# Performance work log

Hardware: AMD Instinct MI355X
Metric: run time of the kernel (lower is better)

The kernel has to match this reference:

```python
import jax, jax.numpy as jnp
import numpy as np

N = 100000      # nodes
E = 3200000     # edges (avg degree 32)
F_IN = 512      # node features
H = 256         # hidden width (channels[0])
C = 64          # num_classes
K = 10          # APPNP steps
ALPHA = 0.1     # teleport prob


def setup_inputs() -> dict:
    key = jax.random.key(0)
    k1, k2, k3, k4 = jax.random.split(key, 4)
    x = jax.random.normal(k1, (N, F_IN), dtype=jnp.float32)
    edge_index = jax.random.randint(k2, (2, E), 0, N, dtype=jnp.int32)
    W1 = jax.random.normal(k3, (F_IN, H), dtype=jnp.float32) * (1.0 / np.sqrt(F_IN))
    b1 = jnp.zeros((H,), dtype=jnp.float32)
    W2 = jax.random.normal(k4, (H, C), dtype=jnp.float32) * (1.0 / np.sqrt(H))
    b2 = jnp.zeros((C,), dtype=jnp.float32)
    return {"x": x, "edge_index": edge_index, "W1": W1, "b1": b1, "W2": W2, "b2": b2}


def reference(x, edge_index, W1, b1, W2, b2):
    # MLP encoder (dropout is identity at eval time)
    h = jax.nn.relu(x @ W1 + b1) @ W2 + b2  # [N, C]

    # GCN normalization with added self-loops (PyG APPNP default)
    loops = jnp.arange(N, dtype=edge_index.dtype)
    row = jnp.concatenate([edge_index[0], loops])  # source
    col = jnp.concatenate([edge_index[1], loops])  # target
    deg = jax.ops.segment_sum(jnp.ones_like(col, dtype=h.dtype), col, num_segments=N)
    dinv = jnp.where(deg > 0, jax.lax.rsqrt(deg), 0.0)
    norm = (dinv[row] * dinv[col])[:, None]  # [E+N, 1]

    # APPNP: z_{k+1} = (1-alpha) * A_hat z_k + alpha * h
    z = h
    for _ in range(K):
        msg = z[row] * norm                                   # gather + scale
        agg = jax.ops.segment_sum(msg, col, num_segments=N)   # scatter-add
        z = (1.0 - ALPHA) * agg + ALPHA * h

    return jax.nn.log_softmax(z, axis=1)
```

## Files before the change

kernel.cpp:

```cpp
#include <hip/hip_runtime.h>
#include <hip/hip_bf16.h>

#define F_IN 512
#define H_DIM 256
#define C_DIM 64
#define K_STEPS 10
#define ALPHA 0.1f

typedef __attribute__((ext_vector_type(8))) short bf16x8;
typedef __attribute__((ext_vector_type(4))) float f32x4;

static __device__ __forceinline__ ushort f2bf(float f) {
    __hip_bfloat16 b = __float2bfloat16(f);
    return *(ushort*)&b;
}
static __device__ __forceinline__ float bflo(unsigned int w) {
    union { unsigned int i; float f; } v; v.i = w << 16; return v.f;
}
static __device__ __forceinline__ float bfhi(unsigned int w) {
    union { unsigned int i; float f; } v; v.i = w & 0xffff0000u; return v.f;
}

#define ACC8(u) do { \
    acc[0] += bflo(u.x); acc[1] += bfhi(u.x); \
    acc[2] += bflo(u.y); acc[3] += bfhi(u.y); \
    acc[4] += bflo(u.z); acc[5] += bfhi(u.z); \
    acc[6] += bflo(u.w); acc[7] += bfhi(u.w); } while (0)

__global__ void prep_kernel(const float* __restrict__ W1, ushort* __restrict__ W1p,
                            const float* __restrict__ W2, ushort* __restrict__ W2p,
                            int* __restrict__ cnt, int n)
{
    const int o = blockIdx.x * 256 + threadIdx.x;
    {
        const int j = o & 7;
        const int l = (o >> 3) & 63;
        const int b = o >> 9;
        const int f = b & 15, ks = b >> 4;
        const int k = ks * 32 + (l >> 4) * 8 + j;
        const int col = f * 16 + (l & 15);
        W1p[o] = f2bf(W1[k * H_DIM + col]);
    }
    if (o < 16384) {
        const int j = o & 7;
        const int l = (o >> 3) & 63;
        const int b = o >> 9;
        const int f = b & 3, kk = b >> 2;
        const int k = kk * 32 + (l >> 4) * 8 + j;
        const int col = f * 16 + (l & 15);
        W2p[o] = f2bf(W2[k * C_DIM + col]);
    }
    if (o < n) cnt[o] = 0;
}

__global__ void rank_kernel(const int* __restrict__ col, int* __restrict__ cnt,
                            int* __restrict__ rank, int e)
{
    int i = blockIdx.x * 256 + threadIdx.x;
    if (i < e) rank[i] = atomicAdd(&cnt[col[i]], 1);
}

__global__ __launch_bounds__(256) void scan1_kernel(
    const int* __restrict__ cnt, int* __restrict__ rowptr, int* __restrict__ sums,
    float* __restrict__ dinv, int n)
{
    __shared__ int lds[256];
    const int t = threadIdx.x;
    const int base = blockIdx.x * 1024 + t * 4;
    int v[4];
    #pragma unroll
    for (int j = 0; j < 4; ++j) v[j] = (base + j < n) ? cnt[base + j] : 0;
    const int tsum = v[0] + v[1] + v[2] + v[3];
    lds[t] = tsum;
    __syncthreads();
    for (int o = 1; o < 256; o <<= 1) {
        const int add = (t >= o) ? lds[t - o] : 0;
        __syncthreads();
        lds[t] += add;
        __syncthreads();
    }
    int run = lds[t] - tsum;
    #pragma unroll
    for (int j = 0; j < 4; ++j) {
        if (base + j < n) {
            rowptr[base + j] = run;
            dinv[base + j] = rsqrtf((float)v[j] + 1.0f);
        }
        run += v[j];
    }
    if (t == 255) sums[blockIdx.x] = lds[255];
}

__global__ __launch_bounds__(128) void scan2_kernel(int* __restrict__ sums, int nc)
{
    __shared__ int lds[128];
    const int t = threadIdx.x;
    const int v = (t < nc) ? sums[t] : 0;
    lds[t] = v;
    __syncthreads();
    for (int o = 1; o < 128; o <<= 1) {
        const int add = (t >= o) ? lds[t - o] : 0;
        __syncthreads();
        lds[t] += add;
        __syncthreads();
    }
    if (t < nc) sums[t] = lds[t] - v;
}

__global__ void scan3_kernel(int* __restrict__ rowptr, const int* __restrict__ sums, int n, int e)
{
    int i = blockIdx.x * 256 + threadIdx.x;
    if (i < n) rowptr[i] += sums[i >> 10];
    else if (i == n) rowptr[n] = e;
}

__global__ void fill_kernel(const int* __restrict__ row, const int* __restrict__ col,
                            const int* __restrict__ rowptr, const int* __restrict__ rank,
                            int* __restrict__ csr_src, int e)
{
    int i = blockIdx.x * 256 + threadIdx.x;
    if (i < e) csr_src[rowptr[col[i]] + rank[i]] = row[i];
}

__global__ __launch_bounds__(256) void mlp_mfma_kernel(
    const float* __restrict__ x,
    const ushort* __restrict__ W1p, const float* __restrict__ b1,
    const ushort* __restrict__ W2p, const float* __restrict__ b2,
    const float* __restrict__ dinv,
    ushort* __restrict__ ah, ushort* __restrict__ zs, int n)
{
    __shared__ __align__(16) short h1s[4][16 * 264];

    const int t = threadIdx.x;
    const int lane = t & 63;
    const int wv = t >> 6;
    const int ln15 = lane & 15;
    const int hi = lane >> 4;
    const long row0 = (long)blockIdx.x * 64 + wv * 16;

    long arow = row0 + ln15;
    if (arow > (long)n - 1) arow = n - 1;
    const float4* xp = (const float4*)(x + arow * F_IN);

    f32x4 acc[16];
    #pragma unroll
    for (int f = 0; f < 16; ++f) acc[f] = (f32x4){0.f, 0.f, 0.f, 0.f};

    float4 xb[2][2];
    xb[0][0] = xp[hi * 2];     xb[0][1] = xp[hi * 2 + 1];
    xb[1][0] = xp[8 + hi * 2]; xb[1][1] = xp[8 + hi * 2 + 1];

    #pragma unroll
    for (int ks = 0; ks < 16; ++ks) {
        const int sl = ks & 1;
        const float4 a0 = xb[sl][0];
        const float4 a1 = xb[sl][1];
        if (ks + 2 < 16) {
            xb[sl][0] = xp[(ks + 2) * 8 + hi * 2];
            xb[sl][1] = xp[(ks + 2) * 8 + hi * 2 + 1];
        }
        bf16x8 af;
        af[0] = (short)f2bf(a0.x); af[1] = (short)f2bf(a0.y);
        af[2] = (short)f2bf(a0.z); af[3] = (short)f2bf(a0.w);
        af[4] = (short)f2bf(a1.x); af[5] = (short)f2bf(a1.y);
        af[6] = (short)f2bf(a1.z); af[7] = (short)f2bf(a1.w);
        const ushort* wb = W1p + (long)ks * 8192 + lane * 8;
        #pragma unroll
        for (int f = 0; f < 16; ++f) {
            const bf16x8 bfv = *(const bf16x8*)(wb + f * 512);
            acc[f] = __builtin_amdgcn_mfma_f32_16x16x32_bf16(af, bfv, acc[f], 0, 0, 0);
        }
    }

    short* hb = h1s[wv];
    #pragma unroll
    for (int f = 0; f < 16; ++f) {
        const int col = f * 16 + ln15;
        const float bias = b1[col];
        #pragma unroll
        for (int v = 0; v < 4; ++v) {
            float val = acc[f][v] + bias;
            val = val > 0.f ? val : 0.f;
            hb[(hi * 4 + v) * 264 + col] = (short)f2bf(val);
        }
    }

    f32x4 acc2[4];
    #pragma unroll
    for (int f = 0; f < 4; ++f) acc2[f] = (f32x4){0.f, 0.f, 0.f, 0.f};
    #pragma unroll
    for (int kk = 0; kk < 8; ++kk) {
        const bf16x8 a2 = *(const bf16x8*)&hb[ln15 * 264 + kk * 32 + hi * 8];
        #pragma unroll
        for (int f = 0; f < 4; ++f) {
            const bf16x8 b2f = *(const bf16x8*)&W2p[(kk * 4 + f) * 512 + lane * 8];
            acc2[f] = __builtin_amdgcn_mfma_f32_16x16x32_bf16(a2, b2f, acc2[f], 0, 0, 0);
        }
    }

    float di4[4];
    #pragma unroll
    for (int v = 0; v < 4; ++v) {
        const long r = row0 + hi * 4 + v;
        di4[v] = (r < n) ? dinv[r] : 0.f;
    }
    #pragma unroll
    for (int f = 0; f < 4; ++f) {
        const int col = f * 16 + ln15;
        const float bias = b2[col];
        #pragma unroll
        for (int v = 0; v < 4; ++v) {
            const long r = row0 + hi * 4 + v;
            if (r < n) {
                const float val = acc2[f][v] + bias;
                ah[r * C_DIM + col] = f2bf(ALPHA * val);
                zs[r * C_DIM + col] = f2bf(val * di4[v]);
            }
        }
    }
}

__global__ __launch_bounds__(256) void gather8_kernel(
    const int* __restrict__ rowptr, const int* __restrict__ csr_src,
    const float* __restrict__ dinv, const ushort* __restrict__ ah,
    const ushort* __restrict__ zs_in, ushort* __restrict__ zs_out,
    float* __restrict__ out, int n, int final_it)
{
    const int node = (blockIdx.x * 256 + threadIdx.x) >> 6;
    if (node >= n) return;
    const int lane = threadIdx.x & 63;
    const int s = lane >> 3;
    const int cg = lane & 7;

    const int p0 = rowptr[node];
    const int p1 = rowptr[node + 1];

    float acc[8];
    #pragma unroll
    for (int c = 0; c < 8; ++c) acc[c] = 0.f;

    if (s == 0) {
        const uint4 u = *(const uint4*)&zs_in[(long)node * C_DIM + cg * 8];
        ACC8(u);
    }

    if (p0 < p1) {
        int p = p0 + s;
        int c0 = (p     < p1) ? csr_src[p]     : -1;
        int c1 = (p + 8 < p1) ? csr_src[p + 8] : -1;
        while (c0 >= 0) {
            uint4 u0, u1;
            u0 = *(const uint4*)&zs_in[(long)c0 * C_DIM + cg * 8];
            if (c1 >= 0) u1 = *(const uint4*)&zs_in[(long)c1 * C_DIM + cg * 8];
            const int np = p + 16;
            const int n0 = (np     < p1) ? csr_src[np]     : -1;
            const int n1 = (np + 8 < p1) ? csr_src[np + 8] : -1;
            ACC8(u0);
            if (c1 >= 0) ACC8(u1);
            c0 = n0; c1 = n1; p = np;
        }
    }

    #pragma unroll
    for (int c = 0; c < 8; ++c) {
        acc[c] += __shfl_xor(acc[c], 8, 64);
        acc[c] += __shfl_xor(acc[c], 16, 64);
        acc[c] += __shfl_xor(acc[c], 32, 64);
    }

    if (s == 0) {
        const float di = dinv[node];
        const long off = (long)node * C_DIM + cg * 8;
        const uint4 ua = *(const uint4*)&ah[off];
        const float w = (1.0f - ALPHA) * di;
        float z[8];
        z[0] = w * acc[0] + bflo(ua.x);
        z[1] = w * acc[1] + bfhi(ua.x);
        z[2] = w * acc[2] + bflo(ua.y);
        z[3] = w * acc[3] + bfhi(ua.y);
        z[4] = w * acc[4] + bflo(ua.z);
        z[5] = w * acc[5] + bfhi(ua.z);
        z[6] = w * acc[6] + bflo(ua.w);
        z[7] = w * acc[7] + bfhi(ua.w);
        if (!final_it) {
            uint4 o;
            o.x = ((unsigned)f2bf(z[1] * di) << 16) | f2bf(z[0] * di);
            o.y = ((unsigned)f2bf(z[3] * di) << 16) | f2bf(z[2] * di);
            o.z = ((unsigned)f2bf(z[5] * di) << 16) | f2bf(z[4] * di);
            o.w = ((unsigned)f2bf(z[7] * di) << 16) | f2bf(z[6] * di);
            *(uint4*)&zs_out[off] = o;
        } else {
            float m = z[0];
            #pragma unroll
            for (int j = 1; j < 8; ++j) m = fmaxf(m, z[j]);
            m = fmaxf(m, __shfl_xor(m, 1, 64));
            m = fmaxf(m, __shfl_xor(m, 2, 64));
            m = fmaxf(m, __shfl_xor(m, 4, 64));
            float se = 0.f;
            #pragma unroll
            for (int j = 0; j < 8; ++j) se += expf(z[j] - m);
            se += __shfl_xor(se, 1, 64);
            se += __shfl_xor(se, 2, 64);
            se += __shfl_xor(se, 4, 64);
            const float ls = m + logf(se);
            *(float4*)&out[off]     = make_float4(z[0] - ls, z[1] - ls, z[2] - ls, z[3] - ls);
            *(float4*)&out[off + 4] = make_float4(z[4] - ls, z[5] - ls, z[6] - ls, z[7] - ls);
        }
    }
}

extern "C" void kernel_launch(void* const* d_in, const int* in_sizes, int n_in,
                              void* d_out, int out_size, void* d_ws, size_t ws_size,
                              hipStream_t stream)
{
    const float* x  = (const float*)d_in[0];
    const int* ei   = (const int*)d_in[1];
    const float* W1 = (const float*)d_in[2];
    const float* b1 = (const float*)d_in[3];
    const float* W2 = (const float*)d_in[4];
    const float* b2 = (const float*)d_in[5];
    float* out = (float*)d_out;

    const int N = in_sizes[0] / F_IN;
    const int E = in_sizes[1] / 2;
    const int* row = ei;
    const int* col = ei + E;

    ushort* ah     = (ushort*)d_ws;
    ushort* zs_a   = ah + (long)N * C_DIM;
    ushort* zs_b   = zs_a + (long)N * C_DIM;
    float*  dinv   = (float*)(zs_b + (long)N * C_DIM);
    int*    cnt    = (int*)(dinv + N);
    int*    rowptr = cnt + N;
    int*    rank   = rowptr + N + 16;
    int*    csr_src = rank + E;
    int*    sums   = csr_src + E;
    ushort* W1p    = (ushort*)(sums + 128);
    ushort* W2p    = W1p + 131072;

    const int eblk = (E + 255) / 256;
    const int nchunks = (N + 1023) / 1024;

    prep_kernel<<<512, 256, 0, stream>>>(W1, W1p, W2, W2p, cnt, N);

    rank_kernel<<<eblk, 256, 0, stream>>>(col, cnt, rank, E);
    scan1_kernel<<<nchunks, 256, 0, stream>>>(cnt, rowptr, sums, dinv, N);
    scan2_kernel<<<1, 128, 0, stream>>>(sums, nchunks);
    scan3_kernel<<<(N + 256) / 256, 256, 0, stream>>>(rowptr, sums, N, E);
    fill_kernel<<<eblk, 256, 0, stream>>>(row, col, rowptr, rank, csr_src, E);

    mlp_mfma_kernel<<<(N + 63) / 64, 256, 0, stream>>>(x, W1p, b1, W2p, b2,
                                                       dinv, ah, zs_a, N);

    const int gblk = (N + 3) / 4;
    for (int it = 0; it < K_STEPS; ++it) {
        const ushort* in = (it & 1) ? zs_b : zs_a;
        ushort* outb     = (it & 1) ? zs_a : zs_b;
        gather8_kernel<<<gblk, 256, 0, stream>>>(rowptr, csr_src, dinv, ah,
                                                 in, outb, out, N,
                                                 it == K_STEPS - 1 ? 1 : 0);
    }
}
```

Measured before the change: 905.7 us.

## Vectorize CSR build, stage W1 tiles in LDS, deepen gather unroll

The rank and fill kernels now handle four edges per thread with int4 loads, cutting the thread count and load instructions. The MLP kernel streams W1 tiles into double-buffered LDS with global_load_lds and uses an XOR-swizzled layout for the hidden activations, instead of every wave reading W1 from global memory. The x prefetch is dropped, and a barrier per k-step is added. The APPNP gather loop keeps four neighbour rows in flight per lane instead of two, to expose more memory parallelism at the cost of extra registers.

```diff
diff --git a/kernel.cpp b/kernel.cpp
--- a/kernel.cpp
+++ b/kernel.cpp
@@ -26,6 +26,10 @@
     acc[2] += bflo(u.y); acc[3] += bfhi(u.y); \
     acc[4] += bflo(u.z); acc[5] += bfhi(u.z); \
     acc[6] += bflo(u.w); acc[7] += bfhi(u.w); } while (0)
+
+#define GLOAD_LDS16(gp, lp) __builtin_amdgcn_global_load_lds( \
+    (const __attribute__((address_space(1))) unsigned int*)(gp), \
+    (__attribute__((address_space(3))) unsigned int*)(lp), 16, 0, 0)
 
 __global__ void prep_kernel(const float* __restrict__ W1, ushort* __restrict__ W1p,
                             const float* __restrict__ W2, ushort* __restrict__ W2p,
@@ -56,8 +60,17 @@
 __global__ void rank_kernel(const int* __restrict__ col, int* __restrict__ cnt,
                             int* __restrict__ rank, int e)
 {
-    int i = blockIdx.x * 256 + threadIdx.x;
-    if (i < e) rank[i] = atomicAdd(&cnt[col[i]], 1);
+    const int i0 = (blockIdx.x * 256 + threadIdx.x) * 4;
+    if (i0 + 3 < e) {
+        const int4 c = *(const int4*)&col[i0];
+        const int r0 = atomicAdd(&cnt[c.x], 1);
+        const int r1 = atomicAdd(&cnt[c.y], 1);
+        const int r2 = atomicAdd(&cnt[c.z], 1);
+        const int r3 = atomicAdd(&cnt[c.w], 1);
+        *(int4*)&rank[i0] = make_int4(r0, r1, r2, r3);
+    } else {
+        for (int i = i0; i < e; ++i) rank[i] = atomicAdd(&cnt[col[i]], 1);
+    }
 }
 
 __global__ __launch_bounds__(256) void scan1_kernel(
@@ -118,8 +131,18 @@
                             const int* __restrict__ rowptr, const int* __restrict__ rank,
                             int* __restrict__ csr_src, int e)
 {
-    int i = blockIdx.x * 256 + threadIdx.x;
-    if (i < e) csr_src[rowptr[col[i]] + rank[i]] = row[i];
+    const int i0 = (blockIdx.x * 256 + threadIdx.x) * 4;
+    if (i0 + 3 < e) {
+        const int4 c  = *(const int4*)&col[i0];
+        const int4 rk = *(const int4*)&rank[i0];
+        const int4 rw = *(const int4*)&row[i0];
+        csr_src[rowptr[c.x] + rk.x] = rw.x;
+        csr_src[rowptr[c.y] + rk.y] = rw.y;
+        csr_src[rowptr[c.z] + rk.z] = rw.z;
+        csr_src[rowptr[c.w] + rk.w] = rw.w;
+    } else {
+        for (int i = i0; i < e; ++i) csr_src[rowptr[col[i]] + rank[i]] = row[i];
+    }
 }
 
 __global__ __launch_bounds__(256) void mlp_mfma_kernel(
@@ -129,7 +152,7 @@
     const float* __restrict__ dinv,
     ushort* __restrict__ ah, ushort* __restrict__ zs, int n)
 {
-    __shared__ __align__(16) short h1s[4][16 * 264];
+    __shared__ __align__(16) char smem[32768];
 
     const int t = threadIdx.x;
     const int lane = t & 63;
@@ -146,42 +169,53 @@
     #pragma unroll
     for (int f = 0; f < 16; ++f) acc[f] = (f32x4){0.f, 0.f, 0.f, 0.f};
 
-    float4 xb[2][2];
-    xb[0][0] = xp[hi * 2];     xb[0][1] = xp[hi * 2 + 1];
-    xb[1][0] = xp[8 + hi * 2]; xb[1][1] = xp[8 + hi * 2 + 1];
-
-    #pragma unroll
+    {
+        const char* g = (const char*)(W1p);
+        char* l = smem;
+        #pragma unroll
+        for (int j = 0; j < 4; ++j)
+            GLOAD_LDS16(g + j * 4096 + wv * 1024 + lane * 16,
+                        l + j * 4096 + wv * 1024);
+    }
+    __syncthreads();
+
     for (int ks = 0; ks < 16; ++ks) {
-        const int sl = ks & 1;
-        const float4 a0 = xb[sl][0];
-        const float4 a1 = xb[sl][1];
-        if (ks + 2 < 16) {
-            xb[sl][0] = xp[(ks + 2) * 8 + hi * 2];
-            xb[sl][1] = xp[(ks + 2) * 8 + hi * 2 + 1];
-        }
+        if (ks < 15) {
+            const char* g = (const char*)(W1p + (size_t)(ks + 1) * 8192);
+            char* l = smem + ((ks + 1) & 1) * 16384;
+            #pragma unroll
+            for (int j = 0; j < 4; ++j)
+                GLOAD_LDS16(g + j * 4096 + wv * 1024 + lane * 16,
+                            l + j * 4096 + wv * 1024);
+        }
+        const float4 a0 = xp[ks * 8 + hi * 2];
+        const float4 a1 = xp[ks * 8 + hi * 2 + 1];
         bf16x8 af;
         af[0] = (short)f2bf(a0.x); af[1] = (short)f2bf(a0.y);
         af[2] = (short)f2bf(a0.z); af[3] = (short)f2bf(a0.w);
         af[4] = (short)f2bf(a1.x); af[5] = (short)f2bf(a1.y);
         af[6] = (short)f2bf(a1.z); af[7] = (short)f2bf(a1.w);
-        const ushort* wb = W1p + (long)ks * 8192 + lane * 8;
+        const ushort* wb = (const ushort*)(smem + (ks & 1) * 16384) + lane * 8;
         #pragma unroll
         for (int f = 0; f < 16; ++f) {
             const bf16x8 bfv = *(const bf16x8*)(wb + f * 512);
             acc[f] = __builtin_amdgcn_mfma_f32_16x16x32_bf16(af, bfv, acc[f], 0, 0, 0);
         }
-    }
-
-    short* hb = h1s[wv];
+        __syncthreads();
+    }
+
+    char* hreg = smem + wv * 8192;
     #pragma unroll
     for (int f = 0; f < 16; ++f) {
         const int col = f * 16 + ln15;
         const float bias = b1[col];
         #pragma unroll
         for (int v = 0; v < 4; ++v) {
+            const int r = hi * 4 + v;
             float val = acc[f][v] + bias;
             val = val > 0.f ? val : 0.f;
-            hb[(hi * 4 + v) * 264 + col] = (short)f2bf(val);
+            const int pos = (r * 256 + col) * 2;
+            *(short*)(hreg + (pos ^ ((r & 7) << 4))) = (short)f2bf(val);
         }
     }
 
@@ -190,7 +224,8 @@
     for (int f = 0; f < 4; ++f) acc2[f] = (f32x4){0.f, 0.f, 0.f, 0.f};
     #pragma unroll
     for (int kk = 0; kk < 8; ++kk) {
-        const bf16x8 a2 = *(const bf16x8*)&hb[ln15 * 264 + kk * 32 + hi * 8];
+        const int pos = (ln15 * 256 + kk * 32 + hi * 8) * 2;
+        const bf16x8 a2 = *(const bf16x8*)(hreg + (pos ^ ((ln15 & 7) << 4)));
         #pragma unroll
         for (int f = 0; f < 4; ++f) {
             const bf16x8 b2f = *(const bf16x8*)&W2p[(kk * 4 + f) * 512 + lane * 8];
@@ -246,18 +281,26 @@
 
     if (p0 < p1) {
         int p = p0 + s;
-        int c0 = (p     < p1) ? csr_src[p]     : -1;
-        int c1 = (p + 8 < p1) ? csr_src[p + 8] : -1;
+        int c0 = (p      < p1) ? csr_src[p]      : -1;
+        int c1 = (p +  8 < p1) ? csr_src[p +  8] : -1;
+        int c2 = (p + 16 < p1) ? csr_src[p + 16] : -1;
+        int c3 = (p + 24 < p1) ? csr_src[p + 24] : -1;
         while (c0 >= 0) {
-            uint4 u0, u1;
+            uint4 u0, u1, u2, u3;
             u0 = *(const uint4*)&zs_in[(long)c0 * C_DIM + cg * 8];
             if (c1 >= 0) u1 = *(const uint4*)&zs_in[(long)c1 * C_DIM + cg * 8];
-            const int np = p + 16;
-            const int n0 = (np     < p1) ? csr_src[np]     : -1;
-            const int n1 = (np + 8 < p1) ? csr_src[np + 8] : -1;
+            if (c2 >= 0) u2 = *(const uint4*)&zs_in[(long)c2 * C_DIM + cg * 8];
+            if (c3 >= 0) u3 = *(const uint4*)&zs_in[(long)c3 * C_DIM + cg * 8];
+            p += 32;
+            const int n0 = (p      < p1) ? csr_src[p]      : -1;
+            const int n1 = (p +  8 < p1) ? csr_src[p +  8] : -1;
+            const int n2 = (p + 16 < p1) ? csr_src[p + 16] : -1;
+            const int n3 = (p + 24 < p1) ? csr_src[p + 24] : -1;
             ACC8(u0);
             if (c1 >= 0) ACC8(u1);
-            c0 = n0; c1 = n1; p = np;
+            if (c2 >= 0) ACC8(u2);
+            if (c3 >= 0) ACC8(u3);
+            c0 = n0; c1 = n1; c2 = n2; c3 = n3;
         }
     }
 
@@ -327,9 +370,9 @@
     const int* col = ei + E;
 
     ushort* ah     = (ushort*)d_ws;
-    ushort* zs_a   = ah + (long)N * C_DIM;
-    ushort* zs_b   = zs_a + (long)N * C_DIM;
-    float*  dinv   = (float*)(zs_b + (long)N * C_DIM);
+    ushort* zs_a   = ah + (size_t)N * C_DIM;
+    ushort* zs_b   = zs_a + (size_t)N * C_DIM;
+    float*  dinv   = (float*)(zs_b + (size_t)N * C_DIM);
     int*    cnt    = (int*)(dinv + N);
     int*    rowptr = cnt + N;
     int*    rank   = rowptr + N + 16;
@@ -338,16 +381,16 @@
     ushort* W1p    = (ushort*)(sums + 128);
     ushort* W2p    = W1p + 131072;
 
-    const int eblk = (E + 255) / 256;
+    const int eblk4 = (E / 4 + 255) / 256;
     const int nchunks = (N + 1023) / 1024;
 
     prep_kernel<<<512, 256, 0, stream>>>(W1, W1p, W2, W2p, cnt, N);
 
-    rank_kernel<<<eblk, 256, 0, stream>>>(col, cnt, rank, E);
+    rank_kernel<<<eblk4, 256, 0, stream>>>(col, cnt, rank, E);
     scan1_kernel<<<nchunks, 256, 0, stream>>>(cnt, rowptr, sums, dinv, N);
     scan2_kernel<<<1, 128, 0, stream>>>(sums, nchunks);
     scan3_kernel<<<(N + 256) / 256, 256, 0, stream>>>(rowptr, sums, N, E);
-    fill_kernel<<<eblk, 256, 0, stream>>>(row, col, rowptr, rank, csr_src, E);
+    fill_kernel<<<eblk4, 256, 0, stream>>>(row, col, rowptr, rank, csr_src, E);
 
     mlp_mfma_kernel<<<(N + 63) / 64, 256, 0, stream>>>(x, W1p, b1, W2p, b2,
                                                        dinv, ah, zs_a, N);
```

Result: faster. 853.0 us (-5.8%).
